# Kernel optimization log

Hardware: AMD Instinct MI355X
Metric: run time of the kernel (lower is better)

## Reference

```python
import jax, jax.numpy as jnp
import numpy as np

D_MODEL = 1024
N_HEADS = 16
D_K = D_MODEL // N_HEADS


def setup_inputs() -> dict:
    key = jax.random.key(0)
    ks = jax.random.split(key, 12)
    B, S = 2, 2048
    scale = 1.0 / np.sqrt(D_MODEL)
    inp = {
        "q": jax.random.normal(ks[0], (B, S, D_MODEL), jnp.float32),
        "k": jax.random.normal(ks[1], (B, S, D_MODEL), jnp.float32),
        "v": jax.random.normal(ks[2], (B, S, D_MODEL), jnp.float32),
        "k_pe": jax.random.normal(ks[3], (N_HEADS, D_K, S), jnp.float32),
        "Wq": jax.random.normal(ks[4], (D_MODEL, D_MODEL), jnp.float32) * scale,
        "bq": jnp.zeros((D_MODEL,), jnp.float32),
        "Wk": jax.random.normal(ks[5], (D_MODEL, D_MODEL), jnp.float32) * scale,
        "bk": jnp.zeros((D_MODEL,), jnp.float32),
        "Wv": jax.random.normal(ks[6], (D_MODEL, D_MODEL), jnp.float32) * scale,
        "bv": jnp.zeros((D_MODEL,), jnp.float32),
        "Wo": jax.random.normal(ks[7], (D_MODEL, D_MODEL), jnp.float32) * scale,
        "bo": jnp.zeros((D_MODEL,), jnp.float32),
    }
    return inp


def reference(q, k, v, k_pe, Wq, bq, Wk, bk, Wv, bv, Wo, bo):
    B, S, _ = q.shape
    # projections -> [B, H, S, d_k]
    def split_heads(x):
        return x.reshape(B, S, N_HEADS, D_K).transpose(0, 2, 1, 3)
    qh = split_heads(q @ Wq + bq)
    kh = split_heads(k @ Wk + bk)
    vh = split_heads(v @ Wv + bv)
    # content scores + relative positional scores (two matmuls, summed)
    scores = jnp.einsum("bhsd,bhtd->bhst", qh, kh)
    scores = scores + jnp.einsum("bhsd,hdt->bhst", qh, k_pe)
    scores = scores / jnp.sqrt(jnp.asarray(D_K, qh.dtype))
    attn = jax.nn.softmax(scores, axis=-1)
    out = jnp.einsum("bhst,bhtd->bhsd", attn, vh)  # [B,H,S,d_k]
    out = out.transpose(0, 2, 1, 3).reshape(B, S, D_MODEL)
    return out @ Wo + bo
```

## Files before the change

kernel.cpp:

```cpp
#include <hip/hip_runtime.h>
#include <stdint.h>
#include <math.h>

typedef __bf16 bf16;
typedef __attribute__((ext_vector_type(8))) __bf16 bf16x8;
typedef __attribute__((ext_vector_type(4))) __bf16 bf16x4;
typedef __attribute__((ext_vector_type(4))) float f32x4;

#define MFMA_BF16(a, b, c) __builtin_amdgcn_mfma_f32_16x16x32_bf16((a), (b), (c), 0, 0, 0)

#if __has_builtin(__builtin_amdgcn_exp2f)
#define EXP2F __builtin_amdgcn_exp2f
#else
#define EXP2F exp2f
#endif

#define QSCALE 0.18033688011112042f

__device__ __forceinline__ void gl_lds16(const bf16* g, bf16* l) {
  __builtin_amdgcn_global_load_lds(
      (__attribute__((address_space(1))) unsigned int*)(uintptr_t)(g),
      (__attribute__((address_space(3))) unsigned int*)(l),
      16, 0, 0);
}

__global__ __launch_bounds__(256) void prep(
    const float* __restrict__ q, const float* __restrict__ k,
    const float* __restrict__ v, bf16* __restrict__ qb,
    bf16* __restrict__ kb, bf16* __restrict__ vb,
    const float* __restrict__ W0, const float* __restrict__ W1,
    const float* __restrict__ W2, const float* __restrict__ W3,
    bf16* __restrict__ Wt)
{
  __shared__ float tile[64][65];
  const int tid = threadIdx.x;
  const int bid = blockIdx.x;
  if (bid < 6144) {
    const int z = bid >> 11;
    const int idx = bid & 2047;
    const float* s = (z == 0) ? q : (z == 1) ? k : v;
    bf16* d = (z == 0) ? qb : (z == 1) ? kb : vb;
    size_t i = ((size_t)idx * 256 + tid) * 8;
    float4 a = *(const float4*)(s + i);
    float4 b = *(const float4*)(s + i + 4);
    bf16x8 o;
    o[0] = (bf16)a.x; o[1] = (bf16)a.y; o[2] = (bf16)a.z; o[3] = (bf16)a.w;
    o[4] = (bf16)b.x; o[5] = (bf16)b.y; o[6] = (bf16)b.z; o[7] = (bf16)b.w;
    *(bf16x8*)(d + i) = o;
  } else {
    const int t = bid - 6144;
    const int z = t >> 8;
    const int rem = t & 255;
    const int r0 = (rem >> 4) * 64, c0 = (rem & 15) * 64;
    const float* src = (z == 0) ? W0 : (z == 1) ? W1 : (z == 2) ? W2 : W3;
    bf16* dst = Wt + (size_t)z * (1024 * 1024);
#pragma unroll
    for (int h = 0; h < 2; ++h) {
      int qq = tid + h * 256;
      int row = qq >> 3, cc = qq & 7;
      float4 a = *(const float4*)(src + (size_t)(r0 + row) * 1024 + c0 + cc * 8);
      float4 b = *(const float4*)(src + (size_t)(r0 + row) * 1024 + c0 + cc * 8 + 4);
      tile[row][cc * 8 + 0] = a.x; tile[row][cc * 8 + 1] = a.y;
      tile[row][cc * 8 + 2] = a.z; tile[row][cc * 8 + 3] = a.w;
      tile[row][cc * 8 + 4] = b.x; tile[row][cc * 8 + 5] = b.y;
      tile[row][cc * 8 + 6] = b.z; tile[row][cc * 8 + 7] = b.w;
    }
    __syncthreads();
#pragma unroll
    for (int h = 0; h < 2; ++h) {
      int qq = tid + h * 256;
      int row = qq >> 3, cc = qq & 7;
      bf16x8 o;
#pragma unroll
      for (int e = 0; e < 8; ++e) o[e] = (bf16)tile[cc * 8 + e][row];
      *(bf16x8*)(dst + (size_t)(c0 + row) * 1024 + r0 + cc * 8) = o;
    }
  }
}

template <int MODE>
__device__ __forceinline__ void gemm_body(
    const bf16* __restrict__ A, const bf16* __restrict__ Wt,
    const float* __restrict__ bias, float oscale, void* __restrict__ out_v)
{
  __shared__ __align__(16) bf16 As[128 * 32];
  __shared__ __align__(16) bf16 Bs[128 * 32];
  const int tid = threadIdx.x;
  const int w = tid >> 6, lane = tid & 63;
  const int lm = lane & 15, quad = lane >> 4;
  const int wr = w >> 1, wc = w & 1;
  const int m0 = blockIdx.y * 128, n0 = blockIdx.x * 128;

  f32x4 zero4 = {0.f, 0.f, 0.f, 0.f};
  f32x4 acc[4][4];
#pragma unroll
  for (int i = 0; i < 4; ++i)
#pragma unroll
    for (int j = 0; j < 4; ++j) acc[i][j] = zero4;

  for (int kb = 0; kb < 32; ++kb) {
    __syncthreads();
#pragma unroll
    for (int h = 0; h < 2; ++h) {
      int qq = tid + h * 256;
      int row = qq >> 2, cs = qq & 3;
      int cc = cs ^ ((row >> 1) & 3);
      gl_lds16(A + (size_t)(m0 + row) * 1024 + kb * 32 + cc * 8, As + qq * 8);
      gl_lds16(Wt + (size_t)(n0 + row) * 1024 + kb * 32 + cc * 8, Bs + qq * 8);
    }
    __syncthreads();

    bf16x8 af[4], bfv[4];
#pragma unroll
    for (int i = 0; i < 4; ++i) {
      int row = wr * 64 + i * 16 + lm;
      af[i] = *(const bf16x8*)(As + row * 32 + ((quad ^ ((row >> 1) & 3)) * 8));
    }
#pragma unroll
    for (int j = 0; j < 4; ++j) {
      int row = wc * 64 + j * 16 + lm;
      bfv[j] = *(const bf16x8*)(Bs + row * 32 + ((quad ^ ((row >> 1) & 3)) * 8));
    }
#pragma unroll
    for (int i = 0; i < 4; ++i)
#pragma unroll
      for (int j = 0; j < 4; ++j)
        acc[i][j] = MFMA_BF16(af[i], bfv[j], acc[i][j]);
  }

  const int ncol = n0 + wc * 64;
  float bv4[4];
#pragma unroll
  for (int j = 0; j < 4; ++j) bv4[j] = bias[ncol + j * 16 + lm];
#pragma unroll
  for (int i = 0; i < 4; ++i) {
#pragma unroll
    for (int j = 0; j < 4; ++j) {
      const int ng = ncol + j * 16 + lm;
      const int hh = ng >> 6, d = ng & 63;
#pragma unroll
      for (int r = 0; r < 4; ++r) {
        const int mg = m0 + wr * 64 + i * 16 + quad * 4 + r;
        const int b = mg >> 11, s = mg & 2047;
        float val = acc[i][j][r] + bv4[j];
        if (MODE == 0) {
          ((bf16*)out_v)[(((size_t)(b * 16 + hh)) * 2048 + s) * 64 + d] =
              (bf16)(val * oscale);
        } else {
          ((float*)out_v)[(size_t)mg * 1024 + ng] = val;
        }
      }
    }
  }
}

__global__ __launch_bounds__(256) void qkv_gemm(
    const bf16* __restrict__ qb, const bf16* __restrict__ kb, const bf16* __restrict__ vb,
    const bf16* __restrict__ Wt, const float* __restrict__ biq,
    const float* __restrict__ bik, const float* __restrict__ biv,
    bf16* __restrict__ Qs, bf16* __restrict__ Ks, bf16* __restrict__ Vrow)
{
  const int z = blockIdx.z;
  if (z == 0) {
    gemm_body<0>(qb, Wt, biq, QSCALE, Qs);
  } else if (z == 1) {
    gemm_body<0>(kb, Wt + (size_t)1 * 1024 * 1024, bik, 1.f, Ks);
  } else {
    gemm_body<0>(vb, Wt + (size_t)2 * 1024 * 1024, biv, 1.f, Vrow);
  }
}

__global__ __launch_bounds__(256) void out_gemm(
    const bf16* __restrict__ A, const bf16* __restrict__ Wt,
    const float* __restrict__ bias, float* __restrict__ out)
{
  gemm_body<3>(A, Wt, bias, 1.f, out);
}

__global__ __launch_bounds__(256) void post_kv(
    const float* __restrict__ kpe, bf16* __restrict__ Ks,
    const bf16* __restrict__ Vrow, bf16* __restrict__ Vts)
{
  const int tid = threadIdx.x;
  const int bh = blockIdx.y;
  const int t0 = blockIdx.x * 64;
  if (blockIdx.z == 0) {
    __shared__ float tile[64][65];
    const int h = bh & 15;
    const float* src = kpe + (size_t)h * 64 * 2048;
#pragma unroll
    for (int p = 0; p < 2; ++p) {
      int qq = tid + p * 256;
      int d = qq >> 3, cs = qq & 7;
      float4 a = *(const float4*)(src + (size_t)d * 2048 + t0 + cs * 8);
      float4 b = *(const float4*)(src + (size_t)d * 2048 + t0 + cs * 8 + 4);
      tile[d][cs * 8 + 0] = a.x; tile[d][cs * 8 + 1] = a.y;
      tile[d][cs * 8 + 2] = a.z; tile[d][cs * 8 + 3] = a.w;
      tile[d][cs * 8 + 4] = b.x; tile[d][cs * 8 + 5] = b.y;
      tile[d][cs * 8 + 6] = b.z; tile[d][cs * 8 + 7] = b.w;
    }
    __syncthreads();
    bf16* krow = Ks + (size_t)bh * 2048 * 64;
#pragma unroll
    for (int p = 0; p < 2; ++p) {
      int qq = tid + p * 256;
      int t = qq >> 3, cs = qq & 7;
      bf16x8 kv = *(const bf16x8*)(krow + (size_t)(t0 + t) * 64 + cs * 8);
      bf16x8 o;
#pragma unroll
      for (int e = 0; e < 8; ++e) o[e] = (bf16)((float)kv[e] + tile[cs * 8 + e][t]);
      *(bf16x8*)(krow + (size_t)(t0 + t) * 64 + cs * 8) = o;
    }
  } else {
    __shared__ bf16 btile[64][72];
    const bf16* src = Vrow + (size_t)bh * 2048 * 64;
#pragma unroll
    for (int p = 0; p < 2; ++p) {
      int qq = tid + p * 256;
      int t = qq >> 3, cs = qq & 7;
      *(bf16x8*)(&btile[t][cs * 8]) =
          *(const bf16x8*)(src + (size_t)(t0 + t) * 64 + cs * 8);
    }
    __syncthreads();
    bf16* dst = Vts + (size_t)bh * 64 * 2048;
#pragma unroll
    for (int p = 0; p < 2; ++p) {
      int qq = tid + p * 256;
      int d = qq >> 3, cs = qq & 7;
      bf16x8 o;
#pragma unroll
      for (int e = 0; e < 8; ++e) o[e] = btile[cs * 8 + e][d];
      *(bf16x8*)(dst + (size_t)d * 2048 + t0 + cs * 8) = o;
    }
  }
}

__global__ __launch_bounds__(512) void flash_attn(
    const bf16* __restrict__ Q, const bf16* __restrict__ K,
    const bf16* __restrict__ Vt, bf16* __restrict__ O)
{
  __shared__ __align__(16) bf16 Qt[128 * 64];
  __shared__ __align__(16) bf16 Kt[64 * 64];
  __shared__ __align__(16) bf16 Vs[64 * 64];
  __shared__ __align__(16) bf16 Ps[128 * 72];

  const int tid = threadIdx.x;
  const int w = tid >> 6, lane = tid & 63;
  const int lm = lane & 15, quad = lane >> 4;
  const int bh = blockIdx.y;
  const int s0 = blockIdx.x * 128;
  const size_t qkbase = (size_t)bh * (2048 * 64);
  const size_t vbase = (size_t)bh * (64 * 2048);

#pragma unroll
  for (int h = 0; h < 2; ++h) {
    int qq = tid + h * 512;
    int row = qq >> 3, cs = qq & 7;
    int cc = cs ^ (row & 7);
    gl_lds16(Q + qkbase + (size_t)(s0 + row) * 64 + cc * 8, Qt + qq * 8);
  }
  __syncthreads();

  bf16x8 qa0, qa1;
  {
    int row = w * 16 + lm;
    qa0 = *(const bf16x8*)(Qt + row * 64 + ((quad ^ (row & 7)) * 8));
    qa1 = *(const bf16x8*)(Qt + row * 64 + (((quad + 4) ^ (row & 7)) * 8));
  }

  f32x4 zero4 = {0.f, 0.f, 0.f, 0.f};
  float l_part = 0.f;
  f32x4 oacc[4];
#pragma unroll
  for (int dt = 0; dt < 4; ++dt) oacc[dt] = zero4;

  const int prow = (w * 16 + lm) * 72;

  for (int kt = 0; kt < 32; ++kt) {
    const int t0 = kt * 64;
    __syncthreads();
    {
      int row = tid >> 3, cs = tid & 7;
      int cc = cs ^ (row & 7);
      gl_lds16(K + qkbase + (size_t)(t0 + row) * 64 + cc * 8, Kt + tid * 8);
      gl_lds16(Vt + vbase + (size_t)row * 2048 + t0 + cc * 8, Vs + tid * 8);
    }
    __syncthreads();

#pragma unroll
    for (int c = 0; c < 4; ++c) {
      int row = c * 16 + lm;
      bf16x8 kb0 = *(const bf16x8*)(Kt + row * 64 + ((quad ^ (row & 7)) * 8));
      bf16x8 kb1 = *(const bf16x8*)(Kt + row * 64 + (((quad + 4) ^ (row & 7)) * 8));
      f32x4 z = MFMA_BF16(kb0, qa0, zero4);
      f32x4 st = MFMA_BF16(kb1, qa1, z);
      bf16x4 pk;
#pragma unroll
      for (int r = 0; r < 4; ++r) {
        float p = EXP2F(st[r]);
        l_part += p;
        pk[r] = (bf16)p;
      }
      *(bf16x4*)(Ps + prow + c * 16 + quad * 4) = pk;
    }

    bf16x8 pa0 = *(const bf16x8*)(Ps + prow + quad * 8);
    bf16x8 pa1 = *(const bf16x8*)(Ps + prow + 32 + quad * 8);
#pragma unroll
    for (int dt = 0; dt < 4; ++dt) {
      int row = dt * 16 + lm;
      bf16x8 va0 = *(const bf16x8*)(Vs + row * 64 + ((quad ^ (row & 7)) * 8));
      bf16x8 va1 = *(const bf16x8*)(Vs + row * 64 + (((quad + 4) ^ (row & 7)) * 8));
      oacc[dt] = MFMA_BF16(va0, pa0, oacc[dt]);
      oacc[dt] = MFMA_BF16(va1, pa1, oacc[dt]);
    }
  }

  float l = l_part;
  l += __shfl_xor(l, 16, 64);
  l += __shfl_xor(l, 32, 64);
  float inv = 1.f / l;
#pragma unroll
  for (int dt = 0; dt < 4; ++dt)
#pragma unroll
    for (int r = 0; r < 4; ++r)
      Ps[prow + dt * 16 + quad * 4 + r] = (bf16)(oacc[dt][r] * inv);

  const int b = bh >> 4, hh = bh & 15;
  const int srow = s0 + w * 16 + lm;
  const size_t ob = ((size_t)(b * 2048 + srow)) * 1024 + hh * 64;
#pragma unroll
  for (int half = 0; half < 2; ++half) {
    bf16x8 ov = *(const bf16x8*)(Ps + prow + (half * 4 + quad) * 8);
    *(bf16x8*)(O + ob + (half * 4 + quad) * 8) = ov;
  }
}

extern "C" void kernel_launch(void* const* d_in, const int* in_sizes, int n_in,
                              void* d_out, int out_size, void* d_ws, size_t ws_size,
                              hipStream_t stream) {
  (void)in_sizes; (void)n_in; (void)out_size; (void)ws_size;
  const float* q   = (const float*)d_in[0];
  const float* k   = (const float*)d_in[1];
  const float* v   = (const float*)d_in[2];
  const float* kpe = (const float*)d_in[3];
  const float* Wq  = (const float*)d_in[4];
  const float* bq  = (const float*)d_in[5];
  const float* Wk  = (const float*)d_in[6];
  const float* bk  = (const float*)d_in[7];
  const float* Wv  = (const float*)d_in[8];
  const float* bv  = (const float*)d_in[9];
  const float* Wo  = (const float*)d_in[10];
  const float* bo  = (const float*)d_in[11];

  const size_t NT = 4u * 1024 * 1024;
  bf16* ws  = (bf16*)d_ws;
  bf16* Wt  = ws;
  bf16* qb  = Wt + NT;
  bf16* kb  = qb + NT;
  bf16* vb  = kb + NT;
  bf16* Qs  = vb + NT;
  bf16* Ks  = Qs + NT;
  bf16* Vts = Ks + NT;
  bf16* Oa  = Vts + NT;
  bf16* Vrow = Oa;

  prep<<<dim3(7168), 256, 0, stream>>>(q, k, v, qb, kb, vb, Wq, Wk, Wv, Wo, Wt);
  qkv_gemm<<<dim3(8, 32, 3), 256, 0, stream>>>(qb, kb, vb, Wt, bq, bk, bv,
                                               Qs, Ks, Vrow);
  post_kv<<<dim3(32, 32, 2), 256, 0, stream>>>(kpe, Ks, Vrow, Vts);
  flash_attn<<<dim3(16, 32), 512, 0, stream>>>(Qs, Ks, Vts, Oa);
  out_gemm<<<dim3(8, 32), 256, 0, stream>>>(Oa, Wt + 3u * 1024 * 1024, bo,
                                            (float*)d_out);
}
```

Measured before the change: 241.4 us.

## Fuse k_pe add and V transpose into QKV GEMM epilogue; widen flash-attn warps

Removes the post_kv kernel. The K projection epilogue now adds k_pe directly, and the V projection writes transposed V straight from the GEMM by swapping the MFMA operand order. The GEMM epilogue is also changed to emit vectorized bf16x4 and float4 stores. Flash attention drops to 256 threads, with each warp handling two 16-row query groups so K and V fragments are reused across them; this cuts a kernel launch and an intermediate round trip but raises register pressure and lowers per-block parallelism.

New measurement: 250.3 us. 1.04x slower.

```diff
diff --git a/kernel.cpp b/kernel.cpp
--- a/kernel.cpp
+++ b/kernel.cpp
@@ -81,14 +81,15 @@
 template <int MODE>
 __device__ __forceinline__ void gemm_body(
     const bf16* __restrict__ A, const bf16* __restrict__ Wt,
-    const float* __restrict__ bias, float oscale, void* __restrict__ out_v)
+    const float* __restrict__ bias, const float* __restrict__ kpe,
+    void* __restrict__ out_v)
 {
   __shared__ __align__(16) bf16 As[128 * 32];
   __shared__ __align__(16) bf16 Bs[128 * 32];
   const int tid = threadIdx.x;
   const int w = tid >> 6, lane = tid & 63;
   const int lm = lane & 15, quad = lane >> 4;
-  const int wr = w >> 1, wc = w & 1;
+  const int wm = w >> 1, wn = w & 1;
   const int m0 = blockIdx.y * 128, n0 = blockIdx.x * 128;
 
   f32x4 zero4 = {0.f, 0.f, 0.f, 0.f};
@@ -110,44 +111,72 @@
     }
     __syncthreads();
 
-    bf16x8 af[4], bfv[4];
+    bf16x8 af[4], wf[4];
+#pragma unroll
+    for (int j = 0; j < 4; ++j) {
+      int row = wm * 64 + j * 16 + lm;
+      af[j] = *(const bf16x8*)(As + row * 32 + ((quad ^ ((row >> 1) & 3)) * 8));
+    }
 #pragma unroll
     for (int i = 0; i < 4; ++i) {
-      int row = wr * 64 + i * 16 + lm;
-      af[i] = *(const bf16x8*)(As + row * 32 + ((quad ^ ((row >> 1) & 3)) * 8));
-    }
-#pragma unroll
-    for (int j = 0; j < 4; ++j) {
-      int row = wc * 64 + j * 16 + lm;
-      bfv[j] = *(const bf16x8*)(Bs + row * 32 + ((quad ^ ((row >> 1) & 3)) * 8));
+      int row = wn * 64 + i * 16 + lm;
+      wf[i] = *(const bf16x8*)(Bs + row * 32 + ((quad ^ ((row >> 1) & 3)) * 8));
     }
 #pragma unroll
     for (int i = 0; i < 4; ++i)
 #pragma unroll
-      for (int j = 0; j < 4; ++j)
-        acc[i][j] = MFMA_BF16(af[i], bfv[j], acc[i][j]);
-  }
-
-  const int ncol = n0 + wc * 64;
-  float bv4[4];
-#pragma unroll
-  for (int j = 0; j < 4; ++j) bv4[j] = bias[ncol + j * 16 + lm];
-#pragma unroll
-  for (int i = 0; i < 4; ++i) {
-#pragma unroll
-    for (int j = 0; j < 4; ++j) {
-      const int ng = ncol + j * 16 + lm;
+      for (int j = 0; j < 4; ++j) {
+        if (MODE == 2)
+          acc[i][j] = MFMA_BF16(af[j], wf[i], acc[i][j]);
+        else
+          acc[i][j] = MFMA_BF16(wf[i], af[j], acc[i][j]);
+      }
+  }
+
+  if (MODE == 2) {
+#pragma unroll
+    for (int i = 0; i < 4; ++i) {
+      const int ng = n0 + wn * 64 + i * 16 + lm;
       const int hh = ng >> 6, d = ng & 63;
-#pragma unroll
-      for (int r = 0; r < 4; ++r) {
-        const int mg = m0 + wr * 64 + i * 16 + quad * 4 + r;
+      const float bv = bias[ng];
+#pragma unroll
+      for (int j = 0; j < 4; ++j) {
+        const int mg = m0 + wm * 64 + j * 16 + quad * 4;
         const int b = mg >> 11, s = mg & 2047;
-        float val = acc[i][j][r] + bv4[j];
-        if (MODE == 0) {
-          ((bf16*)out_v)[(((size_t)(b * 16 + hh)) * 2048 + s) * 64 + d] =
-              (bf16)(val * oscale);
+        bf16x4 o;
+#pragma unroll
+        for (int r = 0; r < 4; ++r) o[r] = (bf16)(acc[i][j][r] + bv);
+        *(bf16x4*)((bf16*)out_v +
+                   (((size_t)(b * 16 + hh)) * 64 + d) * 2048 + s) = o;
+      }
+    }
+  } else {
+#pragma unroll
+    for (int i = 0; i < 4; ++i) {
+      const int nb = n0 + wn * 64 + i * 16 + quad * 4;
+      const float4 bv4 = *(const float4*)(bias + nb);
+      const int hh = nb >> 6, db = nb & 63;
+#pragma unroll
+      for (int j = 0; j < 4; ++j) {
+        const int mg = m0 + wm * 64 + j * 16 + lm;
+        const int b = mg >> 11, s = mg & 2047;
+        if (MODE == 3) {
+          float4 o;
+          o.x = acc[i][j][0] + bv4.x; o.y = acc[i][j][1] + bv4.y;
+          o.z = acc[i][j][2] + bv4.z; o.w = acc[i][j][3] + bv4.w;
+          *(float4*)((float*)out_v + (size_t)mg * 1024 + nb) = o;
         } else {
-          ((float*)out_v)[(size_t)mg * 1024 + ng] = val;
+          bf16x4 o;
+#pragma unroll
+          for (int r = 0; r < 4; ++r) {
+            float val = acc[i][j][r] + ((const float*)&bv4)[r];
+            if (MODE == 0) val *= QSCALE;
+            if (MODE == 1)
+              val += kpe[((size_t)(hh * 64 + db + r)) * 2048 + s];
+            o[r] = (bf16)val;
+          }
+          *(bf16x4*)((bf16*)out_v +
+                     (((size_t)(b * 16 + hh)) * 2048 + s) * 64 + db) = o;
         }
       }
     }
@@ -158,15 +187,16 @@
     const bf16* __restrict__ qb, const bf16* __restrict__ kb, const bf16* __restrict__ vb,
     const bf16* __restrict__ Wt, const float* __restrict__ biq,
     const float* __restrict__ bik, const float* __restrict__ biv,
-    bf16* __restrict__ Qs, bf16* __restrict__ Ks, bf16* __restrict__ Vrow)
+    const float* __restrict__ kpe,
+    bf16* __restrict__ Qs, bf16* __restrict__ Ks, bf16* __restrict__ Vts)
 {
   const int z = blockIdx.z;
   if (z == 0) {
-    gemm_body<0>(qb, Wt, biq, QSCALE, Qs);
+    gemm_body<0>(qb, Wt, biq, nullptr, Qs);
   } else if (z == 1) {
-    gemm_body<0>(kb, Wt + (size_t)1 * 1024 * 1024, bik, 1.f, Ks);
+    gemm_body<1>(kb, Wt + (size_t)1 * 1024 * 1024, bik, kpe, Ks);
   } else {
-    gemm_body<0>(vb, Wt + (size_t)2 * 1024 * 1024, biv, 1.f, Vrow);
+    gemm_body<2>(vb, Wt + (size_t)2 * 1024 * 1024, biv, nullptr, Vts);
   }
 }
 
@@ -174,75 +204,19 @@
     const bf16* __restrict__ A, const bf16* __restrict__ Wt,
     const float* __restrict__ bias, float* __restrict__ out)
 {
-  gemm_body<3>(A, Wt, bias, 1.f, out);
-}
-
-__global__ __launch_bounds__(256) void post_kv(
-    const float* __restrict__ kpe, bf16* __restrict__ Ks,
-    const bf16* __restrict__ Vrow, bf16* __restrict__ Vts)
-{
-  const int tid = threadIdx.x;
-  const int bh = blockIdx.y;
-  const int t0 = blockIdx.x * 64;
-  if (blockIdx.z == 0) {
-    __shared__ float tile[64][65];
-    const int h = bh & 15;
-    const float* src = kpe + (size_t)h * 64 * 2048;
-#pragma unroll
-    for (int p = 0; p < 2; ++p) {
-      int qq = tid + p * 256;
-      int d = qq >> 3, cs = qq & 7;
-      float4 a = *(const float4*)(src + (size_t)d * 2048 + t0 + cs * 8);
-      float4 b = *(const float4*)(src + (size_t)d * 2048 + t0 + cs * 8 + 4);
-      tile[d][cs * 8 + 0] = a.x; tile[d][cs * 8 + 1] = a.y;
-      tile[d][cs * 8 + 2] = a.z; tile[d][cs * 8 + 3] = a.w;
-      tile[d][cs * 8 + 4] = b.x; tile[d][cs * 8 + 5] = b.y;
-      tile[d][cs * 8 + 6] = b.z; tile[d][cs * 8 + 7] = b.w;
-    }
-    __syncthreads();
-    bf16* krow = Ks + (size_t)bh * 2048 * 64;
-#pragma unroll
-    for (int p = 0; p < 2; ++p) {
-      int qq = tid + p * 256;
-      int t = qq >> 3, cs = qq & 7;
-      bf16x8 kv = *(const bf16x8*)(krow + (size_t)(t0 + t) * 64 + cs * 8);
-      bf16x8 o;
-#pragma unroll
-      for (int e = 0; e < 8; ++e) o[e] = (bf16)((float)kv[e] + tile[cs * 8 + e][t]);
-      *(bf16x8*)(krow + (size_t)(t0 + t) * 64 + cs * 8) = o;
-    }
-  } else {
-    __shared__ bf16 btile[64][72];
-    const bf16* src = Vrow + (size_t)bh * 2048 * 64;
-#pragma unroll
-    for (int p = 0; p < 2; ++p) {
-      int qq = tid + p * 256;
-      int t = qq >> 3, cs = qq & 7;
-      *(bf16x8*)(&btile[t][cs * 8]) =
-          *(const bf16x8*)(src + (size_t)(t0 + t) * 64 + cs * 8);
-    }
-    __syncthreads();
-    bf16* dst = Vts + (size_t)bh * 64 * 2048;
-#pragma unroll
-    for (int p = 0; p < 2; ++p) {
-      int qq = tid + p * 256;
-      int d = qq >> 3, cs = qq & 7;
-      bf16x8 o;
-#pragma unroll
-      for (int e = 0; e < 8; ++e) o[e] = btile[cs * 8 + e][d];
-      *(bf16x8*)(dst + (size_t)d * 2048 + t0 + cs * 8) = o;
-    }
-  }
-}
-
-__global__ __launch_bounds__(512) void flash_attn(
+  gemm_body<3>(A, Wt, bias, nullptr, out);
+}
+
+#define PST 76
+
+__global__ __launch_bounds__(256) void flash_attn(
     const bf16* __restrict__ Q, const bf16* __restrict__ K,
     const bf16* __restrict__ Vt, bf16* __restrict__ O)
 {
   __shared__ __align__(16) bf16 Qt[128 * 64];
   __shared__ __align__(16) bf16 Kt[64 * 64];
   __shared__ __align__(16) bf16 Vs[64 * 64];
-  __shared__ __align__(16) bf16 Ps[128 * 72];
+  __shared__ __align__(16) bf16 Ps[128 * PST];
 
   const int tid = threadIdx.x;
   const int w = tid >> 6, lane = tid & 63;
@@ -253,37 +227,42 @@
   const size_t vbase = (size_t)bh * (64 * 2048);
 
 #pragma unroll
-  for (int h = 0; h < 2; ++h) {
-    int qq = tid + h * 512;
+  for (int h = 0; h < 4; ++h) {
+    int qq = tid + h * 256;
     int row = qq >> 3, cs = qq & 7;
     int cc = cs ^ (row & 7);
     gl_lds16(Q + qkbase + (size_t)(s0 + row) * 64 + cc * 8, Qt + qq * 8);
   }
   __syncthreads();
 
-  bf16x8 qa0, qa1;
-  {
-    int row = w * 16 + lm;
-    qa0 = *(const bf16x8*)(Qt + row * 64 + ((quad ^ (row & 7)) * 8));
-    qa1 = *(const bf16x8*)(Qt + row * 64 + (((quad + 4) ^ (row & 7)) * 8));
+  bf16x8 qa[2][2];
+#pragma unroll
+  for (int g = 0; g < 2; ++g) {
+    int row = w * 32 + g * 16 + lm;
+    qa[g][0] = *(const bf16x8*)(Qt + row * 64 + ((quad ^ (row & 7)) * 8));
+    qa[g][1] = *(const bf16x8*)(Qt + row * 64 + (((quad + 4) ^ (row & 7)) * 8));
   }
 
   f32x4 zero4 = {0.f, 0.f, 0.f, 0.f};
-  float l_part = 0.f;
-  f32x4 oacc[4];
-#pragma unroll
-  for (int dt = 0; dt < 4; ++dt) oacc[dt] = zero4;
-
-  const int prow = (w * 16 + lm) * 72;
+  float l_part[2] = {0.f, 0.f};
+  f32x4 oacc[2][4];
+#pragma unroll
+  for (int g = 0; g < 2; ++g)
+#pragma unroll
+    for (int dt = 0; dt < 4; ++dt) oacc[g][dt] = zero4;
+
+  const int prow[2] = {(w * 32 + lm) * PST, (w * 32 + 16 + lm) * PST};
 
   for (int kt = 0; kt < 32; ++kt) {
     const int t0 = kt * 64;
     __syncthreads();
-    {
-      int row = tid >> 3, cs = tid & 7;
+#pragma unroll
+    for (int h = 0; h < 2; ++h) {
+      int qq = tid + h * 256;
+      int row = qq >> 3, cs = qq & 7;
       int cc = cs ^ (row & 7);
-      gl_lds16(K + qkbase + (size_t)(t0 + row) * 64 + cc * 8, Kt + tid * 8);
-      gl_lds16(Vt + vbase + (size_t)row * 2048 + t0 + cc * 8, Vs + tid * 8);
+      gl_lds16(K + qkbase + (size_t)(t0 + row) * 64 + cc * 8, Kt + qq * 8);
+      gl_lds16(Vt + vbase + (size_t)row * 2048 + t0 + cc * 8, Vs + qq * 8);
     }
     __syncthreads();
 
@@ -292,47 +271,60 @@
       int row = c * 16 + lm;
       bf16x8 kb0 = *(const bf16x8*)(Kt + row * 64 + ((quad ^ (row & 7)) * 8));
       bf16x8 kb1 = *(const bf16x8*)(Kt + row * 64 + (((quad + 4) ^ (row & 7)) * 8));
-      f32x4 z = MFMA_BF16(kb0, qa0, zero4);
-      f32x4 st = MFMA_BF16(kb1, qa1, z);
-      bf16x4 pk;
-#pragma unroll
-      for (int r = 0; r < 4; ++r) {
-        float p = EXP2F(st[r]);
-        l_part += p;
-        pk[r] = (bf16)p;
-      }
-      *(bf16x4*)(Ps + prow + c * 16 + quad * 4) = pk;
-    }
-
-    bf16x8 pa0 = *(const bf16x8*)(Ps + prow + quad * 8);
-    bf16x8 pa1 = *(const bf16x8*)(Ps + prow + 32 + quad * 8);
+#pragma unroll
+      for (int g = 0; g < 2; ++g) {
+        f32x4 z = MFMA_BF16(kb0, qa[g][0], zero4);
+        f32x4 st = MFMA_BF16(kb1, qa[g][1], z);
+        bf16x4 pk;
+#pragma unroll
+        for (int r = 0; r < 4; ++r) {
+          float p = EXP2F(st[r]);
+          l_part[g] += p;
+          pk[r] = (bf16)p;
+        }
+        *(bf16x4*)(Ps + prow[g] + c * 16 + quad * 4) = pk;
+      }
+    }
+
+    bf16x8 pa[2][2];
+#pragma unroll
+    for (int g = 0; g < 2; ++g) {
+      pa[g][0] = *(const bf16x8*)(Ps + prow[g] + quad * 8);
+      pa[g][1] = *(const bf16x8*)(Ps + prow[g] + 32 + quad * 8);
+    }
 #pragma unroll
     for (int dt = 0; dt < 4; ++dt) {
       int row = dt * 16 + lm;
       bf16x8 va0 = *(const bf16x8*)(Vs + row * 64 + ((quad ^ (row & 7)) * 8));
       bf16x8 va1 = *(const bf16x8*)(Vs + row * 64 + (((quad + 4) ^ (row & 7)) * 8));
-      oacc[dt] = MFMA_BF16(va0, pa0, oacc[dt]);
-      oacc[dt] = MFMA_BF16(va1, pa1, oacc[dt]);
-    }
-  }
-
-  float l = l_part;
-  l += __shfl_xor(l, 16, 64);
-  l += __shfl_xor(l, 32, 64);
-  float inv = 1.f / l;
-#pragma unroll
-  for (int dt = 0; dt < 4; ++dt)
-#pragma unroll
-    for (int r = 0; r < 4; ++r)
-      Ps[prow + dt * 16 + quad * 4 + r] = (bf16)(oacc[dt][r] * inv);
+#pragma unroll
+      for (int g = 0; g < 2; ++g) {
+        oacc[g][dt] = MFMA_BF16(va0, pa[g][0], oacc[g][dt]);
+        oacc[g][dt] = MFMA_BF16(va1, pa[g][1], oacc[g][dt]);
+      }
+    }
+  }
 
   const int b = bh >> 4, hh = bh & 15;
-  const int srow = s0 + w * 16 + lm;
-  const size_t ob = ((size_t)(b * 2048 + srow)) * 1024 + hh * 64;
-#pragma unroll
-  for (int half = 0; half < 2; ++half) {
-    bf16x8 ov = *(const bf16x8*)(Ps + prow + (half * 4 + quad) * 8);
-    *(bf16x8*)(O + ob + (half * 4 + quad) * 8) = ov;
+#pragma unroll
+  for (int g = 0; g < 2; ++g) {
+    float l = l_part[g];
+    l += __shfl_xor(l, 16, 64);
+    l += __shfl_xor(l, 32, 64);
+    float inv = 1.f / l;
+#pragma unroll
+    for (int dt = 0; dt < 4; ++dt)
+#pragma unroll
+      for (int r = 0; r < 4; ++r)
+        Ps[prow[g] + dt * 16 + quad * 4 + r] = (bf16)(oacc[g][dt][r] * inv);
+
+    const int srow = s0 + w * 32 + g * 16 + lm;
+    const size_t ob = ((size_t)(b * 2048 + srow)) * 1024 + hh * 64;
+#pragma unroll
+    for (int half = 0; half < 2; ++half) {
+      bf16x8 ov = *(const bf16x8*)(Ps + prow[g] + (half * 4 + quad) * 8);
+      *(bf16x8*)(O + ob + (half * 4 + quad) * 8) = ov;
+    }
   }
 }
 
@@ -363,13 +355,11 @@
   bf16* Ks  = Qs + NT;
   bf16* Vts = Ks + NT;
   bf16* Oa  = Vts + NT;
-  bf16* Vrow = Oa;
 
   prep<<<dim3(7168), 256, 0, stream>>>(q, k, v, qb, kb, vb, Wq, Wk, Wv, Wo, Wt);
-  qkv_gemm<<<dim3(8, 32, 3), 256, 0, stream>>>(qb, kb, vb, Wt, bq, bk, bv,
-                                               Qs, Ks, Vrow);
-  post_kv<<<dim3(32, 32, 2), 256, 0, stream>>>(kpe, Ks, Vrow, Vts);
-  flash_attn<<<dim3(16, 32), 512, 0, stream>>>(Qs, Ks, Vts, Oa);
+  qkv_gemm<<<dim3(8, 32, 3), 256, 0, stream>>>(qb, kb, vb, Wt, bq, bk, bv, kpe,
+                                               Qs, Ks, Vts);
+  flash_attn<<<dim3(16, 32), 256, 0, stream>>>(Qs, Ks, Vts, Oa);
   out_gemm<<<dim3(8, 32), 256, 0, stream>>>(Oa, Wt + 3u * 1024 * 1024, bo,
                                             (float*)d_out);
 }
```
